# Optimization experiments

Measured on AMD Instinct MI355X. Metric: run time of the kernel, lower is better.

Reference implementation:

```python
import jax, jax.numpy as jnp
import numpy as np

N_OUT = 8      # outer experts
INNER = 2      # inner experts per outer expert
E = N_OUT * INNER  # 16 total experts
ACTI = 2       # outer top-k (acti_num)
PATTERN = (2, 1)   # inner top-k per outer slot (acti_pattern)
D = 1024       # hidden_dim
F = 512        # expert ffn dim
B, S = 1, 1024


def setup_inputs() -> dict:
    key = jax.random.key(0)
    ks = jax.random.split(key, 6)
    w = lambda k, shape: jax.random.normal(k, shape, jnp.float32) * 0.02
    return {
        "hidden_states": jax.random.normal(ks[0], (B, S, D), jnp.float32),
        "w_out_gate": w(ks[1], (N_OUT, D)),
        "w_in_gates": w(ks[2], (N_OUT, INNER, D)),
        "w_gate_proj": w(ks[3], (E, F, D)),
        "w_up_proj": w(ks[4], (E, F, D)),
        "w_down_proj": w(ks[5], (E, D, F)),
    }


def reference(hidden_states, w_out_gate, w_in_gates, w_gate_proj, w_up_proj, w_down_proj):
    Bb, Ss, Dd = hidden_states.shape
    x = hidden_states.reshape(-1, Dd)          # [T, D]
    T = x.shape[0]

    # --- RouterCompound: outer gate ---
    logits = x @ w_out_gate.T                  # [T, n_out]
    probs = jax.nn.softmax(logits.astype(jnp.float32), axis=-1)
    rw, sel = jax.lax.top_k(probs, ACTI)       # [T, A] weights, outer expert ids
    rw = rw / rw.sum(axis=-1, keepdims=True)   # norm_topk_prob=True

    # --- inner gates: score all (outer, inner) pairs, gather selected outer ---
    inner_all = jnp.einsum('td,oid->toi', x, w_in_gates)           # [T, n_out, inner]
    inner_sel = jnp.take_along_axis(inner_all, sel[:, :, None], axis=1)  # [T, A, inner]
    max_k = max(PATTERN)
    _, top_idx = jax.lax.top_k(inner_sel, max_k)                   # [T, A, max_k]
    flat_ids = sel[:, :, None] * INNER + top_idx                   # global expert ids
    # per outer slot j keep first PATTERN[j] inner experts (static pattern)
    sel_ids = jnp.concatenate([flat_ids[:, j, :p] for j, p in enumerate(PATTERN)], axis=1)  # [T, K]
    sel_w = jnp.concatenate([jnp.repeat(rw[:, j:j + 1], p, axis=1) for j, p in enumerate(PATTERN)], axis=1)  # [T, K]
    sel_w = sel_w.astype(x.dtype)

    # --- dispatch/combine: dense masked combine (math-identical to index_add loop) ---
    combine = jnp.zeros((T, E), x.dtype).at[jnp.arange(T)[:, None], sel_ids].add(sel_w)  # [T, E]
    g = jnp.einsum('td,efd->tef', x, w_gate_proj)   # [T, E, F]
    u = jnp.einsum('td,efd->tef', x, w_up_proj)
    h = jax.nn.silu(g) * u                          # SwiGLU activation
    y = jnp.einsum('tef,edf->ted', h, w_down_proj)  # [T, E, D]
    out = jnp.einsum('ted,te->td', y, combine)      # weighted combine
    return out.reshape(Bb, Ss, Dd), sel_w
```

## Files before the change

kernel.cpp:

```cpp
#include <hip/hip_runtime.h>
#include <hip/hip_bf16.h>

typedef __bf16 bf16_t;
typedef __bf16 bf16x8 __attribute__((ext_vector_type(8)));
typedef float floatx4 __attribute__((ext_vector_type(4)));
typedef unsigned int u32;

#define T_TOK 1024
#define DIM   1024
#define FF    512
#define NEXP  16

#define FLAG_OFF 0
#define CNT_OFF  64
#define TOK_OFF  256
#define SEL_OFF  65792
#define H_OFF    78080
#define XBF_OFF  (H_OFF + (size_t)3072*512*2)
#define Y_OFF    (XBF_OFF + (size_t)T_TOK*DIM*2)
#define WS_FULL  (Y_OFF + (size_t)3072*DIM*4)

__device__ inline float swiglu(float g, float u) {
    float a = fminf(fmaxf(-g, -60.f), 60.f);
    return g * u / (1.0f + __expf(a));
}

__device__ __forceinline__ void gload_lds16(const void* g, void* l) {
    __builtin_amdgcn_global_load_lds((const __attribute__((address_space(1))) u32*)g,
                                     (__attribute__((address_space(3))) u32*)l, 16, 0, 0);
}

template<int N> __device__ __forceinline__ void waitv() {
    asm volatile("s_waitcnt vmcnt(%0)" :: "n"(N) : "memory");
}
__device__ __forceinline__ void barrier_raw() { __builtin_amdgcn_s_barrier(); }

__device__ __forceinline__ bf16x8 cvt8(float4 a, float4 b) {
    bf16x8 r;
    r[0]=(bf16_t)a.x; r[1]=(bf16_t)a.y; r[2]=(bf16_t)a.z; r[3]=(bf16_t)a.w;
    r[4]=(bf16_t)b.x; r[5]=(bf16_t)b.y; r[6]=(bf16_t)b.z; r[7]=(bf16_t)b.w;
    return r;
}

__device__ __forceinline__ bf16x8 rdA(const char* L, int r, int q) {
    return *(const bf16x8*)(L + r * 128 + ((q ^ (r & 7)) << 4));
}
template<bool F32>
__device__ __forceinline__ bf16x8 rdB(const char* L, int r, int q) {
    if constexpr (F32) {
        const float* p = (const float*)(L + r * 256);
        float4 a = *(const float4*)(p + ((((2*q)    ) ^ (r & 15)) << 2));
        float4 b = *(const float4*)(p + ((((2*q) + 1) ^ (r & 15)) << 2));
        return cvt8(a, b);
    } else {
        return *(const bf16x8*)(L + r * 128 + ((q ^ (r & 7)) << 4));
    }
}

__device__ inline bf16x8 loadB8r(const void* base, size_t off, bool f32) {
    if (f32) {
        const float4* p = (const float4*)((const float*)base + off);
        return cvt8(p[0], p[1]);
    } else {
        return *(const bf16x8*)((const bf16_t*)base + off);
    }
}

__device__ int blk_f32(const void* p, int tid, int* tmp) {
    const unsigned short* h = (const unsigned short*)p;
    unsigned bad = 0;
    for (int i = tid; i < 4096; i += 256) {
        unsigned e = ((unsigned)h[i] >> 7) & 0xFFu;
        if (e >= 0x90u) bad = 1;
    }
    unsigned long long bl = __ballot(bad != 0);
    __syncthreads();
    if ((tid & 63) == 0) tmp[tid >> 6] = (bl != 0ull) ? 1 : 0;
    __syncthreads();
    return tmp[0] | tmp[1] | tmp[2] | tmp[3];
}

__global__ __launch_bounds__(256) void prep_kernel(
    const void* __restrict__ x, const void* __restrict__ w_out, const void* __restrict__ w_in,
    const void* __restrict__ wg, const void* __restrict__ wu, const void* __restrict__ wd,
    float* __restrict__ selw_out, int* __restrict__ sel_ids,
    bf16_t* __restrict__ xb, int* __restrict__ flags)
{
    const int b = blockIdx.x;
    const int tid = threadIdx.x;
    __shared__ int tmp[4];
    __shared__ float Ls[24];

    if (b >= T_TOK) {
        const int j = b - T_TOK;
        const void* ps[6] = {x, w_out, w_in, wg, wu, wd};
        const unsigned short* h = (const unsigned short*)ps[j];
        unsigned bad = 0;
        for (int i = tid; i < 4096; i += 256) {
            unsigned e = ((unsigned)h[i] >> 7) & 0xFFu;
            if (e >= 0x90u) bad = 1;
        }
        unsigned long long bl = __ballot(bad != 0);
        if ((tid & 63) == 0) tmp[tid >> 6] = (bl != 0ull) ? 1 : 0;
        __syncthreads();
        if (tid == 0) flags[j] = tmp[0] | tmp[1] | tmp[2] | tmp[3];
        return;
    }

    const bool xf  = blk_f32(x, tid, tmp) != 0;
    const bool gof = blk_f32(w_out, tid, tmp) != 0;
    const bool gif = blk_f32(w_in, tid, tmp) != 0;

    const int wave = tid >> 6, lane = tid & 63;
    const int t = b;

    float xv[16];
    if (xf) {
        const float* xp = (const float*)x + (size_t)t * DIM;
        #pragma unroll
        for (int i = 0; i < 16; i++) xv[i] = xp[lane + 64 * i];
    } else {
        const bf16_t* xp = (const bf16_t*)x + (size_t)t * DIM;
        #pragma unroll
        for (int i = 0; i < 16; i++) xv[i] = (float)xp[lane + 64 * i];
    }

    if (wave == 0 && xb) {
        #pragma unroll
        for (int i = 0; i < 16; i++)
            xb[(size_t)t * DIM + lane + 64 * i] = (bf16_t)xv[i];
    }

    #pragma unroll
    for (int jj = 0; jj < 6; jj++) {
        const int j = wave * 6 + jj;
        const void* gb; int row; bool gf;
        if (j < 8) { gb = w_out; row = j;     gf = gof; }
        else       { gb = w_in;  row = j - 8; gf = gif; }
        float s = 0.f;
        if (gf) {
            const float* gp = (const float*)gb + (size_t)row * DIM;
            #pragma unroll
            for (int i = 0; i < 16; i++) s += xv[i] * gp[lane + 64 * i];
        } else {
            const bf16_t* gp = (const bf16_t*)gb + (size_t)row * DIM;
            #pragma unroll
            for (int i = 0; i < 16; i++) s += xv[i] * (float)gp[lane + 64 * i];
        }
        #pragma unroll
        for (int m = 32; m >= 1; m >>= 1) s += __shfl_xor(s, m, 64);
        if (lane == 0) Ls[j] = s;
    }
    __syncthreads();

    if (tid == 0) {
        const float* logits = Ls;
        float mx = logits[0];
        for (int o = 1; o < 8; o++) mx = fmaxf(mx, logits[o]);
        float p[8];
        for (int o = 0; o < 8; o++) p[o] = __expf(logits[o] - mx);
        int i0 = 0;
        for (int o = 1; o < 8; o++) if (logits[o] > logits[i0]) i0 = o;
        int i1 = (i0 == 0) ? 1 : 0;
        for (int o = 0; o < 8; o++) if (o != i0 && logits[o] > logits[i1]) i1 = o;
        float rsum = p[i0] + p[i1];
        float rw0 = p[i0] / rsum, rw1 = p[i1] / rsum;

        float a0 = logits[8 + i0 * 2], a1 = logits[8 + i0 * 2 + 1];
        int j00 = (a1 > a0) ? 1 : 0;
        float b0 = logits[8 + i1 * 2], b1 = logits[8 + i1 * 2 + 1];
        int j10 = (b1 > b0) ? 1 : 0;

        int   ids[3] = { i0 * 2 + j00, i0 * 2 + (1 - j00), i1 * 2 + j10 };
        float w[3]   = { rw0, rw0, rw1 };

        #pragma unroll
        for (int k = 0; k < 3; k++) {
            selw_out[t * 3 + k] = w[k];
            sel_ids[t * 3 + k]  = ids[k];
        }
    }
}

__global__ __launch_bounds__(1024) void bin2_kernel(
    const int* __restrict__ sel_ids,
    int* __restrict__ cnt, int* __restrict__ tok_enc)
{
    const int e = blockIdx.x, tid = threadIdx.x;
    const int wave = tid >> 6, lane = tid & 63;
    __shared__ int wbase[16];

    int my = -1;
    #pragma unroll
    for (int k = 0; k < 3; k++) {
        int id = sel_ids[tid * 3 + k];
        if (id == e) my = tid | (k << 16);
    }
    unsigned long long b = __ballot(my >= 0);
    if (lane == 0) wbase[wave] = __popcll(b);
    __syncthreads();
    if (tid == 0) {
        int s = 0;
        for (int w = 0; w < 16; w++) { int c = wbase[w]; wbase[w] = s; s += c; }
        cnt[e] = s;
    }
    __syncthreads();
    if (my >= 0) {
        int pos = wbase[wave] + __popcll(b & ((1ull << lane) - 1ull));
        if (pos < T_TOK) tok_enc[e * T_TOK + pos] = my;
    }
}


template<bool GF, bool UF>
__device__ __forceinline__ void gateup4_body(
    const bf16_t* __restrict__ xb,
    const void* __restrict__ wg, const void* __restrict__ wu,
    const int* __restrict__ cnt, const int* __restrict__ tok_enc,
    bf16_t* __restrict__ H,
    char* Xs, char* Gs, char* Us, int* toks, int* hrow)
{
    const int ft = blockIdx.x, mt = blockIdx.y, e = blockIdx.z;
    int C = cnt[e]; if (C > T_TOK) C = T_TOK; if (C < 0) C = 0;
    if (mt * 128 >= C) return;

    const int tid = threadIdx.x;
    if (tid < 128) {
        int idx = mt * 128 + tid, t = 0, hr = -1;
        if (idx < C) {
            int enc = tok_enc[e * T_TOK + idx];
            int tt = enc & 0xFFFF, kk = (enc >> 16) & 0xFFFF;
            if (tt < T_TOK && kk < 3) { t = tt; hr = tt * 3 + kk; }
        }
        toks[tid] = t; hrow[tid] = hr;
    }
    __syncthreads();

    const int wave = tid >> 6, lane = tid & 63;
    const int mh = wave >> 2, fq = wave & 3;
    const int rsel = lane & 15, kq = lane >> 4;

    constexpr int NC  = 16;
    constexpr int NG  = GF ? 2 : 1;
    constexpr int NU  = UF ? 2 : 1;
    constexpr int PER = 2 + NG + NU;
    constexpr int GSTR = GF ? 16384 : 8192;
    constexpr int USTR = UF ? 16384 : 8192;
    const int wrow0 = e * FF + ft * 64;

    const bf16_t* px[2];
    #pragma unroll
    for (int j = 0; j < 2; j++) {
        int n = (j * 8 + wave) * 64 + lane, r = n >> 3, s = n & 7;
        px[j] = xb + (size_t)toks[r] * DIM + ((s ^ (r & 7)) << 3);
    }
    const float*  pgf[2]; const bf16_t* pgh = nullptr;
    const float*  puf[2]; const bf16_t* puh = nullptr;
    if constexpr (GF) {
        #pragma unroll
        for (int j = 0; j < 2; j++) {
            int n = (j * 8 + wave) * 64 + lane, r = n >> 4, s = n & 15;
            pgf[j] = (const float*)wg + (size_t)(wrow0 + r) * DIM + ((s ^ (r & 15)) << 2);
        }
    } else {
        int n = wave * 64 + lane, r = n >> 3, s = n & 7;
        pgh = (const bf16_t*)wg + (size_t)(wrow0 + r) * DIM + ((s ^ (r & 7)) << 3);
    }
    if constexpr (UF) {
        #pragma unroll
        for (int j = 0; j < 2; j++) {
            int n = (j * 8 + wave) * 64 + lane, r = n >> 4, s = n & 15;
            puf[j] = (const float*)wu + (size_t)(wrow0 + r) * DIM + ((s ^ (r & 15)) << 2);
        }
    } else {
        int n = wave * 64 + lane, r = n >> 3, s = n & 7;
        puh = (const bf16_t*)wu + (size_t)(wrow0 + r) * DIM + ((s ^ (r & 7)) << 3);
    }

    auto issue = [&](int kc) {
        const int buf = kc % 3;
        #pragma unroll
        for (int j = 0; j < 2; j++)
            gload_lds16(px[j] + kc * 64, Xs + buf * 16384 + (j * 8 + wave) * 1024);
        if constexpr (GF) {
            #pragma unroll
            for (int j = 0; j < 2; j++)
                gload_lds16(pgf[j] + kc * 64, Gs + buf * GSTR + (j * 8 + wave) * 1024);
        } else {
            gload_lds16(pgh + kc * 64, Gs + buf * GSTR + wave * 1024);
        }
        if constexpr (UF) {
            #pragma unroll
            for (int j = 0; j < 2; j++)
                gload_lds16(puf[j] + kc * 64, Us + buf * USTR + (j * 8 + wave) * 1024);
        } else {
            gload_lds16(puh + kc * 64, Us + buf * USTR + wave * 1024);
        }
    };

    floatx4 ag[4], au[4];
    #pragma unroll
    for (int ms = 0; ms < 4; ms++) { ag[ms] = (floatx4){0,0,0,0}; au[ms] = (floatx4){0,0,0,0}; }

    issue(0);
    issue(1);

    #pragma unroll
    for (int kc = 0; kc < NC; kc++) {
        if (kc + 2 < NC) issue(kc + 2);
        if (kc + 2 < NC)      waitv<2 * PER>();
        else if (kc + 1 < NC) waitv<PER>();
        else                  waitv<0>();
        barrier_raw();
        __builtin_amdgcn_sched_barrier(0);

        const char* X = Xs + (kc % 3) * 16384;
        const char* G = Gs + (kc % 3) * GSTR;
        const char* U = Us + (kc % 3) * USTR;
        #pragma unroll
        for (int i = 0; i < 2; i++) {
            const int q = i * 4 + kq;
            bf16x8 a[4];
            #pragma unroll
            for (int ms = 0; ms < 4; ms++) a[ms] = rdA(X, mh * 64 + ms * 16 + rsel, q);
            bf16x8 bg = rdB<GF>(G, fq * 16 + rsel, q);
            bf16x8 bu = rdB<UF>(U, fq * 16 + rsel, q);
            #pragma unroll
            for (int ms = 0; ms < 4; ms++) {
                ag[ms] = __builtin_amdgcn_mfma_f32_16x16x32_bf16(a[ms], bg, ag[ms], 0, 0, 0);
                au[ms] = __builtin_amdgcn_mfma_f32_16x16x32_bf16(a[ms], bu, au[ms], 0, 0, 0);
            }
        }
        barrier_raw();
    }

    const int f = ft * 64 + fq * 16 + rsel;
    #pragma unroll
    for (int ms = 0; ms < 4; ms++)
        #pragma unroll
        for (int r = 0; r < 4; r++) {
            int m = mh * 64 + ms * 16 + kq * 4 + r;
            int hr = hrow[m];
            if (hr >= 0)
                H[(size_t)hr * FF + f] = (bf16_t)swiglu(ag[ms][r], au[ms][r]);
        }
}

__global__ __launch_bounds__(512, 1) void gateup4_kernel(
    const bf16_t* __restrict__ xb,
    const void* __restrict__ wg, const void* __restrict__ wu,
    const int* __restrict__ flags, const int* __restrict__ cnt,
    const int* __restrict__ tok_enc, bf16_t* __restrict__ H)
{
    __shared__ __align__(16) char Xs[3 * 16384];
    __shared__ __align__(16) char Gs[3 * 16384];
    __shared__ __align__(16) char Us[3 * 16384];
    __shared__ int toks[128];
    __shared__ int hrow[128];
    const bool gf = flags[3] != 0, uf = flags[4] != 0;
    if (gf) {
        if (uf) gateup4_body<true,  true >(xb, wg, wu, cnt, tok_enc, H, Xs, Gs, Us, toks, hrow);
        else    gateup4_body<true,  false>(xb, wg, wu, cnt, tok_enc, H, Xs, Gs, Us, toks, hrow);
    } else {
        if (uf) gateup4_body<false, true >(xb, wg, wu, cnt, tok_enc, H, Xs, Gs, Us, toks, hrow);
        else    gateup4_body<false, false>(xb, wg, wu, cnt, tok_enc, H, Xs, Gs, Us, toks, hrow);
    }
}

template<bool DF>
__device__ __forceinline__ void down4_body(
    const void* __restrict__ wd,
    const int* __restrict__ cnt, const int* __restrict__ tok_enc,
    const bf16_t* __restrict__ H, float* __restrict__ Y,
    char* Hs, char* Ds, int* hsrc, int* hdst)
{
    const int dt = blockIdx.x, mt = blockIdx.y, e = blockIdx.z;
    int C = cnt[e]; if (C > T_TOK) C = T_TOK; if (C < 0) C = 0;
    if (mt * 128 >= C) return;

    const int tid = threadIdx.x;
    if (tid < 128) {
        int idx = mt * 128 + tid, hr = -1;
        if (idx < C) {
            int enc = tok_enc[e * T_TOK + idx];
            int tt = enc & 0xFFFF, kk = (enc >> 16) & 0xFFFF;
            if (tt < T_TOK && kk < 3) hr = tt * 3 + kk;
        }
        hsrc[tid] = (hr >= 0) ? hr : 0;
        hdst[tid] = hr;
    }
    __syncthreads();

    const int wave = tid >> 6, lane = tid & 63;
    const int mh = wave >> 2, dq = wave & 3;
    const int rsel = lane & 15, kq = lane >> 4;

    constexpr int NC  = 8;
    constexpr int ND  = DF ? 4 : 2;
    constexpr int PER = 2 + ND;
    constexpr int DSTR = DF ? 32768 : 16384;
    const int wrow0 = e * DIM + dt * 128;

    const bf16_t* ph[2];
    #pragma unroll
    for (int j = 0; j < 2; j++) {
        int n = (j * 8 + wave) * 64 + lane, r = n >> 3, s = n & 7;
        ph[j] = H + (size_t)hsrc[r] * FF + ((s ^ (r & 7)) << 3);
    }
    const float*  pdf[4]; const bf16_t* pdh[2];
    if constexpr (DF) {
        #pragma unroll
        for (int j = 0; j < 4; j++) {
            int n = (j * 8 + wave) * 64 + lane, r = n >> 4, s = n & 15;
            pdf[j] = (const float*)wd + (size_t)(wrow0 + r) * FF + ((s ^ (r & 15)) << 2);
        }
    } else {
        #pragma unroll
        for (int j = 0; j < 2; j++) {
            int n = (j * 8 + wave) * 64 + lane, r = n >> 3, s = n & 7;
            pdh[j] = (const bf16_t*)wd + (size_t)(wrow0 + r) * FF + ((s ^ (r & 7)) << 3);
        }
    }

    auto issue = [&](int kc) {
        const int buf = kc % 3;
        #pragma unroll
        for (int j = 0; j < 2; j++)
            gload_lds16(ph[j] + kc * 64, Hs + buf * 16384 + (j * 8 + wave) * 1024);
        if constexpr (DF) {
            #pragma unroll
            for (int j = 0; j < 4; j++)
                gload_lds16(pdf[j] + kc * 64, Ds + buf * DSTR + (j * 8 + wave) * 1024);
        } else {
            #pragma unroll
            for (int j = 0; j < 2; j++)
                gload_lds16(pdh[j] + kc * 64, Ds + buf * DSTR + (j * 8 + wave) * 1024);
        }
    };

    floatx4 acc[4][2];
    #pragma unroll
    for (int ms = 0; ms < 4; ms++)
        #pragma unroll
        for (int nt = 0; nt < 2; nt++) acc[ms][nt] = (floatx4){0,0,0,0};

    issue(0);
    issue(1);

    #pragma unroll
    for (int kc = 0; kc < NC; kc++) {
        if (kc + 2 < NC) issue(kc + 2);
        if (kc + 2 < NC)      waitv<2 * PER>();
        else if (kc + 1 < NC) waitv<PER>();
        else                  waitv<0>();
        barrier_raw();
        __builtin_amdgcn_sched_barrier(0);

        const char* Hb = Hs + (kc % 3) * 16384;
        const char* Db = Ds + (kc % 3) * DSTR;
        #pragma unroll
        for (int i = 0; i < 2; i++) {
            const int q = i * 4 + kq;
            bf16x8 a[4], bd[2];
            #pragma unroll
            for (int ms = 0; ms < 4; ms++) a[ms] = rdA(Hb, mh * 64 + ms * 16 + rsel, q);
            #pragma unroll
            for (int nt = 0; nt < 2; nt++) bd[nt] = rdB<DF>(Db, dq * 32 + nt * 16 + rsel, q);
            #pragma unroll
            for (int ms = 0; ms < 4; ms++)
                #pragma unroll
                for (int nt = 0; nt < 2; nt++)
                    acc[ms][nt] = __builtin_amdgcn_mfma_f32_16x16x32_bf16(a[ms], bd[nt], acc[ms][nt], 0, 0, 0);
        }
        barrier_raw();
    }

    #pragma unroll
    for (int ms = 0; ms < 4; ms++)
        #pragma unroll
        for (int nt = 0; nt < 2; nt++)
            #pragma unroll
            for (int r = 0; r < 4; r++) {
                int m = mh * 64 + ms * 16 + kq * 4 + r;
                int hr = hdst[m];
                if (hr >= 0)
                    Y[(size_t)hr * DIM + dt * 128 + dq * 32 + nt * 16 + rsel] = acc[ms][nt][r];
            }
}

__global__ __launch_bounds__(512, 1) void down4_kernel(
    const void* __restrict__ wd,
    const int* __restrict__ flags, const int* __restrict__ cnt,
    const int* __restrict__ tok_enc,
    const bf16_t* __restrict__ H, float* __restrict__ Y)
{
    __shared__ __align__(16) char Hs[3 * 16384];
    __shared__ __align__(16) char Ds[3 * 32768];
    __shared__ int hsrc[128];
    __shared__ int hdst[128];
    const bool df = flags[5] != 0;
    if (df) down4_body<true >(wd, cnt, tok_enc, H, Y, Hs, Ds, hsrc, hdst);
    else    down4_body<false>(wd, cnt, tok_enc, H, Y, Hs, Ds, hsrc, hdst);
}

__global__ __launch_bounds__(256) void combine_kernel(
    const float* __restrict__ Y, const float* __restrict__ selw,
    float* __restrict__ outp)
{
    int idx = blockIdx.x * 256 + threadIdx.x;
    int t = idx >> 8;
    int d = (idx & 255) * 4;
    float w0 = selw[t * 3 + 0], w1 = selw[t * 3 + 1], w2 = selw[t * 3 + 2];
    float4 y0 = *(const float4*)(Y + (size_t)(t * 3 + 0) * DIM + d);
    float4 y1 = *(const float4*)(Y + (size_t)(t * 3 + 1) * DIM + d);
    float4 y2 = *(const float4*)(Y + (size_t)(t * 3 + 2) * DIM + d);
    float4 o;
    o.x = w0 * y0.x + w1 * y1.x + w2 * y2.x;
    o.y = w0 * y0.y + w1 * y1.y + w2 * y2.y;
    o.z = w0 * y0.z + w1 * y1.z + w2 * y2.z;
    o.w = w0 * y0.w + w1 * y1.w + w2 * y2.w;
    *(float4*)(outp + (size_t)t * DIM + d) = o;
}

__global__ __launch_bounds__(256) void ffn_kernel(
    const void* __restrict__ x,
    const void* __restrict__ wg, const void* __restrict__ wu, const void* __restrict__ wd,
    const int* __restrict__ flags, const int* __restrict__ cnt, const int* __restrict__ tok_enc,
    const float* __restrict__ selw, float* __restrict__ outp)
{
    const int e = blockIdx.x, tile = blockIdx.y;
    int C = cnt[e]; if (C > T_TOK) C = T_TOK; if (C < 0) C = 0;
    if (tile * 16 >= C) return;
    const bool xf = flags[0] != 0, gf = flags[3] != 0, uf = flags[4] != 0, df = flags[5] != 0;

    __shared__ __align__(16) bf16_t Xs[16][1032];
    __shared__ __align__(16) bf16_t Hs[16][520];
    __shared__ int toks[16];
    __shared__ float wts[16];
    const int tid = threadIdx.x;
    if (tid < 16) {
        int idx = tile * 16 + tid, t = -1; float w = 0.f;
        if (idx < C) {
            int enc = tok_enc[e * T_TOK + idx];
            int tt = enc & 0xFFFF, kk = (enc >> 16) & 0xFFFF;
            if (tt < T_TOK && kk < 3) { t = tt; w = selw[tt * 3 + kk]; }
        }
        toks[tid] = t; wts[tid] = w;
    }
    __syncthreads();
    {
        int row = tid >> 4, chunk = tid & 15;
        int t = toks[row];
        bf16x8* dst = (bf16x8*)&Xs[row][chunk * 64];
        if (t >= 0) {
            #pragma unroll
            for (int i = 0; i < 8; i++)
                dst[i] = loadB8r(x, (size_t)t * DIM + chunk * 64 + i * 8, xf);
        } else {
            bf16x8 z;
            #pragma unroll
            for (int kz = 0; kz < 8; kz++) z[kz] = (bf16_t)0.0f;
            #pragma unroll
            for (int i = 0; i < 8; i++) dst[i] = z;
        }
    }
    __syncthreads();

    const int wave = tid >> 6, lane = tid & 63;
    const int rsel = lane & 15, kq = lane >> 4;
    const size_t eoffF = (size_t)e * FF * DIM;
    for (int nt = 0; nt < 8; nt++) {
        const int f0 = wave * 128 + nt * 16;
        const size_t boff = eoffF + (size_t)(f0 + rsel) * DIM + kq * 8;
        const bf16_t* ap = &Xs[rsel][kq * 8];
        floatx4 accg = {0.f,0.f,0.f,0.f};
        floatx4 accu = {0.f,0.f,0.f,0.f};
        for (int k0 = 0; k0 < DIM; k0 += 32) {
            bf16x8 a  = *(const bf16x8*)(ap + k0);
            bf16x8 bg = loadB8r(wg, boff + k0, gf);
            bf16x8 bu = loadB8r(wu, boff + k0, uf);
            accg = __builtin_amdgcn_mfma_f32_16x16x32_bf16(a, bg, accg, 0, 0, 0);
            accu = __builtin_amdgcn_mfma_f32_16x16x32_bf16(a, bu, accu, 0, 0, 0);
        }
        #pragma unroll
        for (int r = 0; r < 4; r++)
            Hs[kq * 4 + r][f0 + rsel] = (bf16_t)swiglu(accg[r], accu[r]);
    }
    __syncthreads();
    const size_t eoffD = (size_t)e * DIM * FF;
    for (int nt = 0; nt < 16; nt++) {
        const int d0 = wave * 256 + nt * 16;
        const size_t boff = eoffD + (size_t)(d0 + rsel) * FF + kq * 8;
        const bf16_t* ap = &Hs[rsel][kq * 8];
        floatx4 acc = {0.f,0.f,0.f,0.f};
        for (int k0 = 0; k0 < FF; k0 += 32) {
            bf16x8 a = *(const bf16x8*)(ap + k0);
            bf16x8 b = loadB8r(wd, boff + k0, df);
            acc = __builtin_amdgcn_mfma_f32_16x16x32_bf16(a, b, acc, 0, 0, 0);
        }
        #pragma unroll
        for (int r = 0; r < 4; r++) {
            int m = kq * 4 + r, t = toks[m];
            if (t >= 0) atomicAdd(outp + (size_t)t * DIM + d0 + rsel, acc[r] * wts[m]);
        }
    }
}

extern "C" void kernel_launch(void* const* d_in, const int* in_sizes, int n_in,
                              void* d_out, int out_size, void* d_ws, size_t ws_size,
                              hipStream_t stream)
{
    const void* x     = d_in[0];
    const void* w_out = d_in[1];
    const void* w_in  = d_in[2];
    const void* wg    = d_in[3];
    const void* wu    = d_in[4];
    const void* wd    = d_in[5];
    float* out  = (float*)d_out;
    float* selw = out + (size_t)T_TOK * DIM;

    char* ws = (char*)d_ws;
    int*    flags = (int*)(ws + FLAG_OFF);
    int*    cnt   = (int*)(ws + CNT_OFF);
    int*    tok   = (int*)(ws + TOK_OFF);
    int*    sel   = (int*)(ws + SEL_OFF);
    bf16_t* H     = (bf16_t*)(ws + H_OFF);
    bf16_t* xbf   = (bf16_t*)(ws + XBF_OFF);
    float*  Y     = (float*)(ws + Y_OFF);

    const bool full = ws_size >= (size_t)WS_FULL;

    if (!full)
        hipMemsetAsync(out, 0, (size_t)T_TOK * DIM * sizeof(float), stream);

    prep_kernel<<<dim3(T_TOK + 6), dim3(256), 0, stream>>>(
        x, w_out, w_in, wg, wu, wd, selw, sel, full ? xbf : (bf16_t*)nullptr, flags);

    bin2_kernel<<<dim3(NEXP), dim3(1024), 0, stream>>>(sel, cnt, tok);

    if (full) {
        gateup4_kernel<<<dim3(8, 8, 16), dim3(512), 0, stream>>>(
            xbf, wg, wu, flags, cnt, tok, H);
        down4_kernel<<<dim3(8, 8, 16), dim3(512), 0, stream>>>(
            wd, flags, cnt, tok, H, Y);
        combine_kernel<<<dim3(T_TOK * DIM / 1024), dim3(256), 0, stream>>>(Y, selw, out);
    } else {
        ffn_kernel<<<dim3(NEXP, 64), dim3(256), 0, stream>>>(
            x, wg, wu, wd, flags, cnt, tok, selw, out);
    }
}
```

Baseline: 201.5 us.

## Pre-convert fp32 expert weights to bf16 and shrink GEMM tiles for occupancy

```diff
diff --git a/kernel.cpp b/kernel.cpp
--- a/kernel.cpp
+++ b/kernel.cpp
@@ -17,7 +17,10 @@
 #define SEL_OFF  65792
 #define H_OFF    78080
 #define XBF_OFF  (H_OFF + (size_t)3072*512*2)
-#define Y_OFF    (XBF_OFF + (size_t)T_TOK*DIM*2)
+#define WGB_OFF  (XBF_OFF + (size_t)T_TOK*DIM*2)
+#define WUB_OFF  (WGB_OFF + (size_t)NEXP*FF*DIM*2)
+#define WDB_OFF  (WUB_OFF + (size_t)NEXP*FF*DIM*2)
+#define Y_OFF    (WDB_OFF + (size_t)NEXP*DIM*FF*2)
 #define WS_FULL  (Y_OFF + (size_t)3072*DIM*4)
 
 __device__ inline float swiglu(float g, float u) {
@@ -42,19 +45,8 @@
     return r;
 }
 
-__device__ __forceinline__ bf16x8 rdA(const char* L, int r, int q) {
+__device__ __forceinline__ bf16x8 rdT(const char* L, int r, int q) {
     return *(const bf16x8*)(L + r * 128 + ((q ^ (r & 7)) << 4));
-}
-template<bool F32>
-__device__ __forceinline__ bf16x8 rdB(const char* L, int r, int q) {
-    if constexpr (F32) {
-        const float* p = (const float*)(L + r * 256);
-        float4 a = *(const float4*)(p + ((((2*q)    ) ^ (r & 15)) << 2));
-        float4 b = *(const float4*)(p + ((((2*q) + 1) ^ (r & 15)) << 2));
-        return cvt8(a, b);
-    } else {
-        return *(const bf16x8*)(L + r * 128 + ((q ^ (r & 7)) << 4));
-    }
 }
 
 __device__ inline bf16x8 loadB8r(const void* base, size_t off, bool f32) {
@@ -80,16 +72,41 @@
     return tmp[0] | tmp[1] | tmp[2] | tmp[3];
 }
 
-__global__ __launch_bounds__(256) void prep_kernel(
+__global__ __launch_bounds__(256) void prep2_kernel(
     const void* __restrict__ x, const void* __restrict__ w_out, const void* __restrict__ w_in,
     const void* __restrict__ wg, const void* __restrict__ wu, const void* __restrict__ wd,
     float* __restrict__ selw_out, int* __restrict__ sel_ids,
-    bf16_t* __restrict__ xb, int* __restrict__ flags)
+    bf16_t* __restrict__ xb, int* __restrict__ flags,
+    bf16_t* __restrict__ wgb, bf16_t* __restrict__ wub, bf16_t* __restrict__ wdb)
 {
     const int b = blockIdx.x;
     const int tid = threadIdx.x;
     __shared__ int tmp[4];
     __shared__ float Ls[24];
+
+    if (b >= T_TOK + 6) {
+        const int c = b - (T_TOK + 6);
+        const int z = c >> 12, i = c & 4095;
+        const void* src; bf16_t* dst;
+        if (z == 0)      { src = wg; dst = wgb; }
+        else if (z == 1) { src = wu; dst = wub; }
+        else             { src = wd; dst = wdb; }
+        const unsigned short* h = (const unsigned short*)src;
+        unsigned bad = 0;
+        for (int k = tid; k < 4096; k += 256) {
+            unsigned ex = ((unsigned)h[k] >> 7) & 0xFFu;
+            if (ex >= 0x90u) bad = 1;
+        }
+        unsigned long long bl = __ballot(bad != 0);
+        if ((tid & 63) == 0) tmp[tid >> 6] = (bl != 0ull) ? 1 : 0;
+        __syncthreads();
+        if (!(tmp[0] | tmp[1] | tmp[2] | tmp[3])) return;
+        size_t off = ((size_t)i * 256 + tid) * 8;
+        const float4* p = (const float4*)((const float*)src + off);
+        float4 a = p[0], bb = p[1];
+        *(bf16x8*)(dst + off) = cvt8(a, bb);
+        return;
+    }
 
     if (b >= T_TOK) {
         const int j = b - T_TOK;
@@ -212,17 +229,25 @@
 }
 
 
-template<bool GF, bool UF>
-__device__ __forceinline__ void gateup4_body(
+__global__ __launch_bounds__(512, 4) void gateup5_kernel(
     const bf16_t* __restrict__ xb,
     const void* __restrict__ wg, const void* __restrict__ wu,
-    const int* __restrict__ cnt, const int* __restrict__ tok_enc,
-    bf16_t* __restrict__ H,
-    char* Xs, char* Gs, char* Us, int* toks, int* hrow)
-{
+    const bf16_t* __restrict__ wgb, const bf16_t* __restrict__ wub,
+    const int* __restrict__ flags, const int* __restrict__ cnt,
+    const int* __restrict__ tok_enc, bf16_t* __restrict__ H)
+{
+    __shared__ __align__(16) char Xs[3 * 16384];
+    __shared__ __align__(16) char Gs[3 * 4096];
+    __shared__ __align__(16) char Us[3 * 4096];
+    __shared__ int toks[128];
+    __shared__ int hrow[128];
+
     const int ft = blockIdx.x, mt = blockIdx.y, e = blockIdx.z;
     int C = cnt[e]; if (C > T_TOK) C = T_TOK; if (C < 0) C = 0;
     if (mt * 128 >= C) return;
+
+    const bf16_t* wgp = (flags[3] != 0) ? wgb : (const bf16_t*)wg;
+    const bf16_t* wup = (flags[4] != 0) ? wub : (const bf16_t*)wu;
 
     const int tid = threadIdx.x;
     if (tid < 128) {
@@ -237,70 +262,38 @@
     __syncthreads();
 
     const int wave = tid >> 6, lane = tid & 63;
-    const int mh = wave >> 2, fq = wave & 3;
+    const int mh = wave >> 1, fq = wave & 1;
     const int rsel = lane & 15, kq = lane >> 4;
 
     constexpr int NC  = 16;
-    constexpr int NG  = GF ? 2 : 1;
-    constexpr int NU  = UF ? 2 : 1;
-    constexpr int PER = 2 + NG + NU;
-    constexpr int GSTR = GF ? 16384 : 8192;
-    constexpr int USTR = UF ? 16384 : 8192;
-    const int wrow0 = e * FF + ft * 64;
+    constexpr int PER = 3;
 
     const bf16_t* px[2];
     #pragma unroll
     for (int j = 0; j < 2; j++) {
-        int n = (j * 8 + wave) * 64 + lane, r = n >> 3, s = n & 7;
+        int n = (2 * wave + j) * 64 + lane, r = n >> 3, s = n & 7;
         px[j] = xb + (size_t)toks[r] * DIM + ((s ^ (r & 7)) << 3);
     }
-    const float*  pgf[2]; const bf16_t* pgh = nullptr;
-    const float*  puf[2]; const bf16_t* puh = nullptr;
-    if constexpr (GF) {
-        #pragma unroll
-        for (int j = 0; j < 2; j++) {
-            int n = (j * 8 + wave) * 64 + lane, r = n >> 4, s = n & 15;
-            pgf[j] = (const float*)wg + (size_t)(wrow0 + r) * DIM + ((s ^ (r & 15)) << 2);
-        }
-    } else {
-        int n = wave * 64 + lane, r = n >> 3, s = n & 7;
-        pgh = (const bf16_t*)wg + (size_t)(wrow0 + r) * DIM + ((s ^ (r & 7)) << 3);
-    }
-    if constexpr (UF) {
-        #pragma unroll
-        for (int j = 0; j < 2; j++) {
-            int n = (j * 8 + wave) * 64 + lane, r = n >> 4, s = n & 15;
-            puf[j] = (const float*)wu + (size_t)(wrow0 + r) * DIM + ((s ^ (r & 15)) << 2);
-        }
-    } else {
-        int n = wave * 64 + lane, r = n >> 3, s = n & 7;
-        puh = (const bf16_t*)wu + (size_t)(wrow0 + r) * DIM + ((s ^ (r & 7)) << 3);
-    }
+    const bf16_t* pw;
+    {
+        int wv = wave & 3;
+        int n = wv * 64 + lane, r = n >> 3, s = n & 7;
+        int row = e * FF + ft * 32 + r;
+        pw = (wave < 4 ? wgp : wup) + (size_t)row * DIM + ((s ^ (r & 7)) << 3);
+    }
+    char* wdst = (wave < 4 ? Gs : Us);
+    const int wslot = (wave & 3) * 1024;
 
     auto issue = [&](int kc) {
         const int buf = kc % 3;
-        #pragma unroll
-        for (int j = 0; j < 2; j++)
-            gload_lds16(px[j] + kc * 64, Xs + buf * 16384 + (j * 8 + wave) * 1024);
-        if constexpr (GF) {
-            #pragma unroll
-            for (int j = 0; j < 2; j++)
-                gload_lds16(pgf[j] + kc * 64, Gs + buf * GSTR + (j * 8 + wave) * 1024);
-        } else {
-            gload_lds16(pgh + kc * 64, Gs + buf * GSTR + wave * 1024);
-        }
-        if constexpr (UF) {
-            #pragma unroll
-            for (int j = 0; j < 2; j++)
-                gload_lds16(puf[j] + kc * 64, Us + buf * USTR + (j * 8 + wave) * 1024);
-        } else {
-            gload_lds16(puh + kc * 64, Us + buf * USTR + wave * 1024);
-        }
+        gload_lds16(px[0] + kc * 64, Xs + buf * 16384 + (2 * wave) * 1024);
+        gload_lds16(px[1] + kc * 64, Xs + buf * 16384 + (2 * wave + 1) * 1024);
+        gload_lds16(pw + kc * 64, wdst + buf * 4096 + wslot);
     };
 
-    floatx4 ag[4], au[4];
-    #pragma unroll
-    for (int ms = 0; ms < 4; ms++) { ag[ms] = (floatx4){0,0,0,0}; au[ms] = (floatx4){0,0,0,0}; }
+    floatx4 ag[2], au[2];
+    #pragma unroll
+    for (int ms = 0; ms < 2; ms++) { ag[ms] = (floatx4){0,0,0,0}; au[ms] = (floatx4){0,0,0,0}; }
 
     issue(0);
     issue(1);
@@ -315,68 +308,51 @@
         __builtin_amdgcn_sched_barrier(0);
 
         const char* X = Xs + (kc % 3) * 16384;
-        const char* G = Gs + (kc % 3) * GSTR;
-        const char* U = Us + (kc % 3) * USTR;
+        const char* G = Gs + (kc % 3) * 4096;
+        const char* U = Us + (kc % 3) * 4096;
         #pragma unroll
         for (int i = 0; i < 2; i++) {
             const int q = i * 4 + kq;
-            bf16x8 a[4];
-            #pragma unroll
-            for (int ms = 0; ms < 4; ms++) a[ms] = rdA(X, mh * 64 + ms * 16 + rsel, q);
-            bf16x8 bg = rdB<GF>(G, fq * 16 + rsel, q);
-            bf16x8 bu = rdB<UF>(U, fq * 16 + rsel, q);
-            #pragma unroll
-            for (int ms = 0; ms < 4; ms++) {
-                ag[ms] = __builtin_amdgcn_mfma_f32_16x16x32_bf16(a[ms], bg, ag[ms], 0, 0, 0);
-                au[ms] = __builtin_amdgcn_mfma_f32_16x16x32_bf16(a[ms], bu, au[ms], 0, 0, 0);
-            }
+            bf16x8 a0 = rdT(X, mh * 32 + rsel, q);
+            bf16x8 a1 = rdT(X, mh * 32 + 16 + rsel, q);
+            bf16x8 bg = rdT(G, fq * 16 + rsel, q);
+            bf16x8 bu = rdT(U, fq * 16 + rsel, q);
+            ag[0] = __builtin_amdgcn_mfma_f32_16x16x32_bf16(a0, bg, ag[0], 0, 0, 0);
+            au[0] = __builtin_amdgcn_mfma_f32_16x16x32_bf16(a0, bu, au[0], 0, 0, 0);
+            ag[1] = __builtin_amdgcn_mfma_f32_16x16x32_bf16(a1, bg, ag[1], 0, 0, 0);
+            au[1] = __builtin_amdgcn_mfma_f32_16x16x32_bf16(a1, bu, au[1], 0, 0, 0);
         }
         barrier_raw();
     }
 
-    const int f = ft * 64 + fq * 16 + rsel;
-    #pragma unroll
-    for (int ms = 0; ms < 4; ms++)
+    const int f = ft * 32 + fq * 16 + rsel;
+    #pragma unroll
+    for (int ms = 0; ms < 2; ms++)
         #pragma unroll
         for (int r = 0; r < 4; r++) {
-            int m = mh * 64 + ms * 16 + kq * 4 + r;
+            int m = mh * 32 + ms * 16 + kq * 4 + r;
             int hr = hrow[m];
             if (hr >= 0)
                 H[(size_t)hr * FF + f] = (bf16_t)swiglu(ag[ms][r], au[ms][r]);
         }
 }
 
-__global__ __launch_bounds__(512, 1) void gateup4_kernel(
-    const bf16_t* __restrict__ xb,
-    const void* __restrict__ wg, const void* __restrict__ wu,
+__global__ __launch_bounds__(512, 4) void down5_kernel(
+    const void* __restrict__ wd, const bf16_t* __restrict__ wdb,
     const int* __restrict__ flags, const int* __restrict__ cnt,
-    const int* __restrict__ tok_enc, bf16_t* __restrict__ H)
-{
-    __shared__ __align__(16) char Xs[3 * 16384];
-    __shared__ __align__(16) char Gs[3 * 16384];
-    __shared__ __align__(16) char Us[3 * 16384];
-    __shared__ int toks[128];
-    __shared__ int hrow[128];
-    const bool gf = flags[3] != 0, uf = flags[4] != 0;
-    if (gf) {
-        if (uf) gateup4_body<true,  true >(xb, wg, wu, cnt, tok_enc, H, Xs, Gs, Us, toks, hrow);
-        else    gateup4_body<true,  false>(xb, wg, wu, cnt, tok_enc, H, Xs, Gs, Us, toks, hrow);
-    } else {
-        if (uf) gateup4_body<false, true >(xb, wg, wu, cnt, tok_enc, H, Xs, Gs, Us, toks, hrow);
-        else    gateup4_body<false, false>(xb, wg, wu, cnt, tok_enc, H, Xs, Gs, Us, toks, hrow);
-    }
-}
-
-template<bool DF>
-__device__ __forceinline__ void down4_body(
-    const void* __restrict__ wd,
-    const int* __restrict__ cnt, const int* __restrict__ tok_enc,
-    const bf16_t* __restrict__ H, float* __restrict__ Y,
-    char* Hs, char* Ds, int* hsrc, int* hdst)
-{
+    const int* __restrict__ tok_enc,
+    const bf16_t* __restrict__ H, float* __restrict__ Y)
+{
+    __shared__ __align__(16) char Hs[3 * 16384];
+    __shared__ __align__(16) char Ds[3 * 8192];
+    __shared__ int hsrc[128];
+    __shared__ int hdst[128];
+
     const int dt = blockIdx.x, mt = blockIdx.y, e = blockIdx.z;
     int C = cnt[e]; if (C > T_TOK) C = T_TOK; if (C < 0) C = 0;
     if (mt * 128 >= C) return;
+
+    const bf16_t* wdp = (flags[5] != 0) ? wdb : (const bf16_t*)wd;
 
     const int tid = threadIdx.x;
     if (tid < 128) {
@@ -392,55 +368,35 @@
     __syncthreads();
 
     const int wave = tid >> 6, lane = tid & 63;
-    const int mh = wave >> 2, dq = wave & 3;
+    const int mh = wave >> 1, dq = wave & 1;
     const int rsel = lane & 15, kq = lane >> 4;
 
     constexpr int NC  = 8;
-    constexpr int ND  = DF ? 4 : 2;
-    constexpr int PER = 2 + ND;
-    constexpr int DSTR = DF ? 32768 : 16384;
-    const int wrow0 = e * DIM + dt * 128;
+    constexpr int PER = 3;
 
     const bf16_t* ph[2];
     #pragma unroll
     for (int j = 0; j < 2; j++) {
-        int n = (j * 8 + wave) * 64 + lane, r = n >> 3, s = n & 7;
+        int n = (2 * wave + j) * 64 + lane, r = n >> 3, s = n & 7;
         ph[j] = H + (size_t)hsrc[r] * FF + ((s ^ (r & 7)) << 3);
     }
-    const float*  pdf[4]; const bf16_t* pdh[2];
-    if constexpr (DF) {
-        #pragma unroll
-        for (int j = 0; j < 4; j++) {
-            int n = (j * 8 + wave) * 64 + lane, r = n >> 4, s = n & 15;
-            pdf[j] = (const float*)wd + (size_t)(wrow0 + r) * FF + ((s ^ (r & 15)) << 2);
-        }
-    } else {
-        #pragma unroll
-        for (int j = 0; j < 2; j++) {
-            int n = (j * 8 + wave) * 64 + lane, r = n >> 3, s = n & 7;
-            pdh[j] = (const bf16_t*)wd + (size_t)(wrow0 + r) * FF + ((s ^ (r & 7)) << 3);
-        }
+    const bf16_t* pd;
+    {
+        int n = wave * 64 + lane, r = n >> 3, s = n & 7;
+        int row = e * DIM + dt * 64 + r;
+        pd = wdp + (size_t)row * FF + ((s ^ (r & 7)) << 3);
     }
 
     auto issue = [&](int kc) {
         const int buf = kc % 3;
-        #pragma unroll
-        for (int j = 0; j < 2; j++)
-            gload_lds16(ph[j] + kc * 64, Hs + buf * 16384 + (j * 8 + wave) * 1024);
-        if constexpr (DF) {
-            #pragma unroll
-            for (int j = 0; j < 4; j++)
-                gload_lds16(pdf[j] + kc * 64, Ds + buf * DSTR + (j * 8 + wave) * 1024);
-        } else {
-            #pragma unroll
-            for (int j = 0; j < 2; j++)
-                gload_lds16(pdh[j] + kc * 64, Ds + buf * DSTR + (j * 8 + wave) * 1024);
-        }
+        gload_lds16(ph[0] + kc * 64, Hs + buf * 16384 + (2 * wave) * 1024);
+        gload_lds16(ph[1] + kc * 64, Hs + buf * 16384 + (2 * wave + 1) * 1024);
+        gload_lds16(pd + kc * 64, Ds + buf * 8192 + wave * 1024);
     };
 
-    floatx4 acc[4][2];
-    #pragma unroll
-    for (int ms = 0; ms < 4; ms++)
+    floatx4 acc[2][2];
+    #pragma unroll
+    for (int ms = 0; ms < 2; ms++)
         #pragma unroll
         for (int nt = 0; nt < 2; nt++) acc[ms][nt] = (floatx4){0,0,0,0};
 
@@ -457,50 +413,33 @@
         __builtin_amdgcn_sched_barrier(0);
 
         const char* Hb = Hs + (kc % 3) * 16384;
-        const char* Db = Ds + (kc % 3) * DSTR;
+        const char* Db = Ds + (kc % 3) * 8192;
         #pragma unroll
         for (int i = 0; i < 2; i++) {
             const int q = i * 4 + kq;
-            bf16x8 a[4], bd[2];
-            #pragma unroll
-            for (int ms = 0; ms < 4; ms++) a[ms] = rdA(Hb, mh * 64 + ms * 16 + rsel, q);
-            #pragma unroll
-            for (int nt = 0; nt < 2; nt++) bd[nt] = rdB<DF>(Db, dq * 32 + nt * 16 + rsel, q);
-            #pragma unroll
-            for (int ms = 0; ms < 4; ms++)
-                #pragma unroll
-                for (int nt = 0; nt < 2; nt++)
-                    acc[ms][nt] = __builtin_amdgcn_mfma_f32_16x16x32_bf16(a[ms], bd[nt], acc[ms][nt], 0, 0, 0);
+            bf16x8 a0 = rdT(Hb, mh * 32 + rsel, q);
+            bf16x8 a1 = rdT(Hb, mh * 32 + 16 + rsel, q);
+            bf16x8 b0 = rdT(Db, dq * 32 + rsel, q);
+            bf16x8 b1 = rdT(Db, dq * 32 + 16 + rsel, q);
+            acc[0][0] = __builtin_amdgcn_mfma_f32_16x16x32_bf16(a0, b0, acc[0][0], 0, 0, 0);
+            acc[0][1] = __builtin_amdgcn_mfma_f32_16x16x32_bf16(a0, b1, acc[0][1], 0, 0, 0);
+            acc[1][0] = __builtin_amdgcn_mfma_f32_16x16x32_bf16(a1, b0, acc[1][0], 0, 0, 0);
+            acc[1][1] = __builtin_amdgcn_mfma_f32_16x16x32_bf16(a1, b1, acc[1][1], 0, 0, 0);
         }
         barrier_raw();
     }
 
     #pragma unroll
-    for (int ms = 0; ms < 4; ms++)
+    for (int ms = 0; ms < 2; ms++)
         #pragma unroll
         for (int nt = 0; nt < 2; nt++)
             #pragma unroll
             for (int r = 0; r < 4; r++) {
-                int m = mh * 64 + ms * 16 + kq * 4 + r;
+                int m = mh * 32 + ms * 16 + kq * 4 + r;
                 int hr = hdst[m];
                 if (hr >= 0)
-                    Y[(size_t)hr * DIM + dt * 128 + dq * 32 + nt * 16 + rsel] = acc[ms][nt][r];
+                    Y[(size_t)hr * DIM + dt * 64 + dq * 32 + nt * 16 + rsel] = acc[ms][nt][r];
             }
-}
-
-__global__ __launch_bounds__(512, 1) void down4_kernel(
-    const void* __restrict__ wd,
-    const int* __restrict__ flags, const int* __restrict__ cnt,
-    const int* __restrict__ tok_enc,
-    const bf16_t* __restrict__ H, float* __restrict__ Y)
-{
-    __shared__ __align__(16) char Hs[3 * 16384];
-    __shared__ __align__(16) char Ds[3 * 32768];
-    __shared__ int hsrc[128];
-    __shared__ int hdst[128];
-    const bool df = flags[5] != 0;
-    if (df) down4_body<true >(wd, cnt, tok_enc, H, Y, Hs, Ds, hsrc, hdst);
-    else    down4_body<false>(wd, cnt, tok_enc, H, Y, Hs, Ds, hsrc, hdst);
 }
 
 __global__ __launch_bounds__(256) void combine_kernel(
@@ -626,6 +565,9 @@
     int*    sel   = (int*)(ws + SEL_OFF);
     bf16_t* H     = (bf16_t*)(ws + H_OFF);
     bf16_t* xbf   = (bf16_t*)(ws + XBF_OFF);
+    bf16_t* wgb   = (bf16_t*)(ws + WGB_OFF);
+    bf16_t* wub   = (bf16_t*)(ws + WUB_OFF);
+    bf16_t* wdb   = (bf16_t*)(ws + WDB_OFF);
     float*  Y     = (float*)(ws + Y_OFF);
 
     const bool full = ws_size >= (size_t)WS_FULL;
@@ -633,16 +575,18 @@
     if (!full)
         hipMemsetAsync(out, 0, (size_t)T_TOK * DIM * sizeof(float), stream);
 
-    prep_kernel<<<dim3(T_TOK + 6), dim3(256), 0, stream>>>(
-        x, w_out, w_in, wg, wu, wd, selw, sel, full ? xbf : (bf16_t*)nullptr, flags);
+    const int nblk = (T_TOK + 6) + (full ? 3 * 4096 : 0);
+    prep2_kernel<<<dim3(nblk), dim3(256), 0, stream>>>(
+        x, w_out, w_in, wg, wu, wd, selw, sel,
+        full ? xbf : (bf16_t*)nullptr, flags, wgb, wub, wdb);
 
     bin2_kernel<<<dim3(NEXP), dim3(1024), 0, stream>>>(sel, cnt, tok);
 
     if (full) {
-        gateup4_kernel<<<dim3(8, 8, 16), dim3(512), 0, stream>>>(
-            xbf, wg, wu, flags, cnt, tok, H);
-        down4_kernel<<<dim3(8, 8, 16), dim3(512), 0, stream>>>(
-            wd, flags, cnt, tok, H, Y);
+        gateup5_kernel<<<dim3(16, 8, 16), dim3(512), 0, stream>>>(
+            xbf, wg, wu, wgb, wub, flags, cnt, tok, H);
+        down5_kernel<<<dim3(16, 8, 16), dim3(512), 0, stream>>>(
+            wd, wdb, flags, cnt, tok, H, Y);
         combine_kernel<<<dim3(T_TOK * DIM / 1024), dim3(256), 0, stream>>>(Y, selw, out);
     } else {
         ffn_kernel<<<dim3(NEXP, 64), dim3(256), 0, stream>>>(
```

Measured after the change: 191.8 us. -4.8%, faster.
